# Optimization experiments

Measured on AMD Instinct MI355X. Metric: run time of the kernel, lower is better.

Reference implementation:

```python
import jax, jax.numpy as jnp
import numpy as np

B, L, DIN = 16, 1024, 512
H, DH = 4, 128          # num_heads = 4, head_dim = in_features // 4
DEG = 16                # avg random in-degree (plus one self-loop per node)
NEG_SLOPE = 0.2         # DGL GATConv default leaky_relu slope


def setup_inputs() -> dict:
    key = jax.random.key(0)
    ks = jax.random.split(key, 8)
    N = B * L
    E = N * DEG
    src = jax.random.randint(ks[0], (E,), 0, N)
    dst = jax.random.randint(ks[1], (E,), 0, N)
    loops = jnp.arange(N)
    src = jnp.concatenate([src, loops])  # self-loops guarantee every dst has in-edges
    dst = jnp.concatenate([dst, loops])
    s = 1.0 / np.sqrt(DIN)
    text = jax.random.normal(ks[2], (B, L, DIN), jnp.float32)
    weight = jax.random.normal(ks[3], (DIN, DIN), jnp.float32) * s      # module's self.weight
    fc_w = jax.random.normal(ks[4], (DIN, H * DH), jnp.float32) * s     # GATConv fc (no bias)
    attn_l = jax.random.normal(ks[5], (H, DH), jnp.float32) * s
    attn_r = jax.random.normal(ks[6], (H, DH), jnp.float32) * s
    bias = jax.random.normal(ks[7], (DIN,), jnp.float32) * 0.01         # module's self.bias
    return {"text": text, "weight": weight, "fc_w": fc_w,
            "attn_l": attn_l, "attn_r": attn_r, "bias": bias,
            "src": src, "dst": dst}


def reference(text, weight, fc_w, attn_l, attn_r, bias, src, dst):
    b, l, d = text.shape
    N = b * l
    # outer linear projection
    hidden = jnp.einsum('bld,de->ble', text, weight)
    feat = hidden.reshape(N, d)
    # GATConv: fc projection to heads
    h = (feat @ fc_w).reshape(N, H, DH)                 # [N, H, DH]
    el = jnp.einsum('nhd,hd->nh', h, attn_l)            # [N, H]
    er = jnp.einsum('nhd,hd->nh', h, attn_r)            # [N, H]
    # edge attention logits (src contributes el, dst contributes er)
    e = jax.nn.leaky_relu(el[src] + er[dst], NEG_SLOPE)  # [E, H]
    # segment (per-destination) softmax, numerically stable
    emax = jax.ops.segment_max(e, dst, num_segments=N)   # [N, H]
    ex = jnp.exp(e - emax[dst])
    denom = jax.ops.segment_sum(ex, dst, num_segments=N)
    alpha = ex / denom[dst]                              # [E, H]
    # weighted message aggregation (scatter-add)
    m = h[src] * alpha[:, :, None]                       # [E, H, DH]
    out = jax.ops.segment_sum(m, dst, num_segments=N)    # [N, H, DH]
    return out.reshape(b, l, H * DH) + bias
```

## Files before the change

kernel.cpp:

```cpp
#include <hip/hip_runtime.h>
#include <stdint.h>

#define AS1 __attribute__((address_space(1)))
#define AS3 __attribute__((address_space(3)))

typedef __attribute__((ext_vector_type(8))) short short8;
typedef __attribute__((ext_vector_type(4))) float f32x4;

#define CAP 64
#define NGEMM 512
#define NSCAT 128

__device__ __forceinline__ short f2bf(float f) {
  union { float f; unsigned u; } v; v.f = f;
  unsigned r = v.u + 0x7fffu + ((v.u >> 16) & 1u);
  return (short)(r >> 16);
}
__device__ __forceinline__ float bf_lo(unsigned w) { union { unsigned u; float f; } v; v.u = w << 16;          return v.f; }
__device__ __forceinline__ float bf_hi(unsigned w) { union { unsigned u; float f; } v; v.u = w & 0xffff0000u;  return v.f; }

__global__ __launch_bounds__(256) void k_w2t(const float* __restrict__ W,
                                             const float* __restrict__ F,
                                             short* __restrict__ W2t,
                                             int* __restrict__ cnt) {
  const int tid = threadIdx.x;
  const int b   = blockIdx.x;
  if (tid < 64) cnt[b * 64 + tid] = 0;

  __shared__ float sW[64][36];
  __shared__ float sF[64][36];
  const int bx = b & 15, by = b >> 4;
  const int d0 = bx * 32, j0 = by * 32;
  const int dx = tid & 15, jy = tid >> 4;
  float a00 = 0.f, a01 = 0.f, a10 = 0.f, a11 = 0.f;
  const int wr = tid >> 3, wc = (tid & 7) * 8;
  const int fr = tid >> 2, fc = (tid & 3) * 8;
  for (int e0 = 0; e0 < 512; e0 += 64) {
    float4 w0 = *(const float4*)&W[(size_t)(d0 + wr) * 512 + e0 + wc];
    float4 w1 = *(const float4*)&W[(size_t)(d0 + wr) * 512 + e0 + wc + 4];
    float4 f0 = *(const float4*)&F[(size_t)(e0 + fr) * 512 + j0 + fc];
    float4 f1 = *(const float4*)&F[(size_t)(e0 + fr) * 512 + j0 + fc + 4];
    sW[wc + 0][wr] = w0.x; sW[wc + 1][wr] = w0.y; sW[wc + 2][wr] = w0.z; sW[wc + 3][wr] = w0.w;
    sW[wc + 4][wr] = w1.x; sW[wc + 5][wr] = w1.y; sW[wc + 6][wr] = w1.z; sW[wc + 7][wr] = w1.w;
    *(float4*)&sF[fr][fc] = f0;
    *(float4*)&sF[fr][fc + 4] = f1;
    __syncthreads();
#pragma unroll
    for (int e = 0; e < 64; ++e) {
      float2 w2 = *(const float2*)&sW[e][dx * 2];
      float2 f2 = *(const float2*)&sF[e][jy * 2];
      a00 += w2.x * f2.x; a01 += w2.x * f2.y;
      a10 += w2.y * f2.x; a11 += w2.y * f2.y;
    }
    __syncthreads();
  }
  short* o0 = W2t + (size_t)(j0 + jy * 2) * 512 + d0 + dx * 2;
  o0[0] = f2bf(a00); o0[1] = f2bf(a10);
  o0[512] = f2bf(a01); o0[513] = f2bf(a11);
}

__global__ __launch_bounds__(256) void k_gemm_scatter(const float* __restrict__ A32,
                                                      const short* __restrict__ Bt,
                                                      short* __restrict__ Cs,
                                                      float* __restrict__ el,
                                                      float* __restrict__ er,
                                                      const float* __restrict__ attn_l,
                                                      const float* __restrict__ attn_r,
                                                      const int* __restrict__ src,
                                                      const int* __restrict__ dst,
                                                      int* __restrict__ cnt,
                                                      int* __restrict__ bucket,
                                                      int E, int N) {
  const int tid = threadIdx.x;
  if (blockIdx.x >= NGEMM) {
    for (int e = (blockIdx.x - NGEMM) * 256 + tid; e < E; e += NSCAT * 256) {
      int d = dst[e];
      int p = atomicAdd(&cnt[d], 1);
      if (p < CAP) bucket[(size_t)d * CAP + p] = src[e];
    }
    return;
  }

  __shared__ __align__(16) short sA[2][128 * 64];
  __shared__ __align__(16) short sB[2][128 * 64];
  __shared__ float sEl[128][2];
  __shared__ float sEr[128][2];
  const int bx   = blockIdx.x;
  const int xcd  = bx & 7, kk = bx >> 3;
  const int bm0  = (xcd * 16 + (kk & 15)) * 128;
  const int hh   = kk >> 4;
  const int bn0  = hh * 128;
  const int lane = tid & 63;
  const int wid  = tid >> 6;
  const int wm   = wid >> 1;
  const int wn   = wid & 1;
  const int cc   = lane & 15;

  f32x4 acc[4][4] = {};

  const int srow  = tid >> 3;
  const int sslot = (tid & 7) ^ (srow & 7);
  const int lslot = tid & 7;
  const int arow  = tid >> 1;
  const int ahalf = tid & 1;

  float4 f[2][8];

#define LOAD_A(SET, KT)                                                              \
  {                                                                                  \
    const float4* gA = (const float4*)(A32 + (size_t)(bm0 + arow) * 512 + (KT) * 64 + ahalf * 32); \
    _Pragma("unroll")                                                                \
    for (int s = 0; s < 8; ++s) f[SET][s] = gA[s];                                   \
  }

#define WRITE_A(SET, BUF)                                                            \
  {                                                                                  \
    _Pragma("unroll")                                                                \
    for (int s = 0; s < 4; ++s) {                                                    \
      short8 v;                                                                      \
      v[0] = f2bf(f[SET][2 * s].x); v[1] = f2bf(f[SET][2 * s].y);                    \
      v[2] = f2bf(f[SET][2 * s].z); v[3] = f2bf(f[SET][2 * s].w);                    \
      v[4] = f2bf(f[SET][2 * s + 1].x); v[5] = f2bf(f[SET][2 * s + 1].y);            \
      v[6] = f2bf(f[SET][2 * s + 1].z); v[7] = f2bf(f[SET][2 * s + 1].w);            \
      int slot = (ahalf * 4 + s) ^ (arow & 7);                                       \
      *(short8*)((BUF) + arow * 64 + slot * 8) = v;                                  \
    }                                                                                \
  }

#define STAGE_B(KT, BUF)                                                             \
  {                                                                                  \
    _Pragma("unroll")                                                                \
    for (int r = 0; r < 4; ++r) {                                                    \
      int row = r * 32 + srow;                                                       \
      __builtin_amdgcn_global_load_lds(                                              \
          (const AS1 void*)(Bt + (size_t)(bn0 + row) * 512 + (KT) * 64 + sslot * 8), \
          (AS3 void*)((BUF) + row * 64 + lslot * 8), 16, 0, 0);                      \
    }                                                                                \
  }

  LOAD_A(0, 0)
  LOAD_A(1, 1)
  STAGE_B(0, sB[0])
  WRITE_A(0, sA[0])
  __syncthreads();

#pragma unroll
  for (int kt = 0; kt < 8; ++kt) {
    const int cur = kt & 1;
    if (kt < 7) STAGE_B(kt + 1, sB[cur ^ 1])
    if (kt < 6) LOAD_A(kt & 1, kt + 2)
#pragma unroll
    for (int ks = 0; ks < 2; ++ks) {
      short8 af[4], bfr[4];
#pragma unroll
      for (int i = 0; i < 4; ++i) {
        int row  = wm * 64 + i * 16 + cc;
        int slot = (ks * 4 + (lane >> 4)) ^ (row & 7);
        af[i] = *(const short8*)(sA[cur] + row * 64 + slot * 8);
      }
#pragma unroll
      for (int j = 0; j < 4; ++j) {
        int row  = wn * 64 + j * 16 + cc;
        int slot = (ks * 4 + (lane >> 4)) ^ (row & 7);
        bfr[j] = *(const short8*)(sB[cur] + row * 64 + slot * 8);
      }
#pragma unroll
      for (int i = 0; i < 4; ++i)
#pragma unroll
        for (int j = 0; j < 4; ++j)
          acc[i][j] = __builtin_amdgcn_mfma_f32_16x16x32_bf16(af[i], bfr[j], acc[i][j], 0, 0, 0);
    }
    if (kt < 7) WRITE_A((kt + 1) & 1, sA[cur ^ 1])
    __syncthreads();
  }

  const int r4 = (lane >> 4) * 4;
#pragma unroll
  for (int i = 0; i < 4; ++i)
#pragma unroll
    for (int j = 0; j < 4; ++j) {
      int cin = wn * 64 + j * 16 + cc;
#pragma unroll
      for (int rg = 0; rg < 4; ++rg) {
        int gr = bm0 + wm * 64 + i * 16 + r4 + rg;
        Cs[((size_t)hh * N + gr) * 128 + cin] = f2bf(acc[i][j][rg]);
      }
    }
  float alv[4], arv[4];
#pragma unroll
  for (int j = 0; j < 4; ++j) {
    int cl = wn * 64 + j * 16 + cc;
    alv[j] = attn_l[hh * 128 + cl];
    arv[j] = attn_r[hh * 128 + cl];
  }
#pragma unroll
  for (int i = 0; i < 4; ++i)
#pragma unroll
    for (int rg = 0; rg < 4; ++rg) {
      float pl = 0.f, pr = 0.f;
#pragma unroll
      for (int j = 0; j < 4; ++j) {
        float v = acc[i][j][rg];
        pl += v * alv[j]; pr += v * arv[j];
      }
#pragma unroll
      for (int d = 1; d < 16; d <<= 1) {
        pl += __shfl_xor(pl, d);
        pr += __shfl_xor(pr, d);
      }
      if (cc == 0) {
        int row = wm * 64 + i * 16 + r4 + rg;
        sEl[row][wn] = pl;
        sEr[row][wn] = pr;
      }
    }
  __syncthreads();
  if (tid < 128) {
    int gr = bm0 + tid;
    el[gr * 4 + hh] = sEl[tid][0] + sEl[tid][1];
    er[gr * 4 + hh] = sEr[tid][0] + sEr[tid][1];
  }
}

__global__ __launch_bounds__(256) void k_aggregate(const int* __restrict__ cnt, const int* __restrict__ bucket,
                                                   const float* __restrict__ el, const float* __restrict__ er,
                                                   const short* __restrict__ hs, const float* __restrict__ bias,
                                                   float* __restrict__ out, int N) {
  const int b    = blockIdx.x;
  const int s    = (b >> 1) & 3;
  const int nt   = (b >> 3) * 2 + (b & 1);
  const int nd   = nt * 4 + (threadIdx.x >> 6);
  const int lane = threadIdx.x & 63;
  const int g    = lane >> 4;
  const int cl   = lane & 15;

  int n = cnt[nd]; n = (n < CAP) ? n : CAP;
  const int* bk = bucket + (size_t)nd * CAP;

  int l   = (lane < n) ? lane : (n - 1);
  int idx = bk[l];
  float ern = er[nd * 4 + s];
  float x = el[idx * 4 + s] + ern;
  x = (x > 0.f) ? x : 0.2f * x;
  float wgt = (lane < n) ? __expf(x) : 0.f;
  float ssum = wgt;
#pragma unroll
  for (int d = 1; d < 64; d <<= 1) ssum += __shfl_xor(ssum, d);

  const short* hbase = hs + (size_t)s * N * 128;
  float acc[8];
#pragma unroll
  for (int j = 0; j < 8; ++j) acc[j] = 0.f;

  for (int base = 0; base < n; base += 8) {
    int e0 = base + g, e1 = base + 4 + g;
    int s0 = __shfl(idx, e0), s1 = __shfl(idx, e1);
    float w0 = __shfl(wgt, e0), w1 = __shfl(wgt, e1);
    uint4 v0 = ((const uint4*)(hbase + (size_t)s0 * 128))[cl];
    uint4 v1 = ((const uint4*)(hbase + (size_t)s1 * 128))[cl];
    acc[0] += w0 * bf_lo(v0.x) + w1 * bf_lo(v1.x);
    acc[1] += w0 * bf_hi(v0.x) + w1 * bf_hi(v1.x);
    acc[2] += w0 * bf_lo(v0.y) + w1 * bf_lo(v1.y);
    acc[3] += w0 * bf_hi(v0.y) + w1 * bf_hi(v1.y);
    acc[4] += w0 * bf_lo(v0.z) + w1 * bf_lo(v1.z);
    acc[5] += w0 * bf_hi(v0.z) + w1 * bf_hi(v1.z);
    acc[6] += w0 * bf_lo(v0.w) + w1 * bf_lo(v1.w);
    acc[7] += w0 * bf_hi(v0.w) + w1 * bf_hi(v1.w);
  }

#pragma unroll
  for (int d = 16; d < 64; d <<= 1) {
#pragma unroll
    for (int j = 0; j < 8; ++j) acc[j] += __shfl_xor(acc[j], d);
  }

  if (g == 0) {
    float inv = 1.f / ssum;
    int c0 = s * 128 + cl * 8;
    float4 b0 = *(const float4*)(bias + c0);
    float4 b1 = *(const float4*)(bias + c0 + 4);
    float4 o0, o1;
    o0.x = acc[0] * inv + b0.x; o0.y = acc[1] * inv + b0.y;
    o0.z = acc[2] * inv + b0.z; o0.w = acc[3] * inv + b0.w;
    o1.x = acc[4] * inv + b1.x; o1.y = acc[5] * inv + b1.y;
    o1.z = acc[6] * inv + b1.z; o1.w = acc[7] * inv + b1.w;
    float* op = out + (size_t)nd * 512 + c0;
    *(float4*)op = o0;
    *(float4*)(op + 4) = o1;
  }
}

extern "C" void kernel_launch(void* const* d_in, const int* in_sizes, int n_in,
                              void* d_out, int out_size, void* d_ws, size_t ws_size,
                              hipStream_t stream) {
  const float* text   = (const float*)d_in[0];
  const float* weight = (const float*)d_in[1];
  const float* fcw    = (const float*)d_in[2];
  const float* attn_l = (const float*)d_in[3];
  const float* attn_r = (const float*)d_in[4];
  const float* bias   = (const float*)d_in[5];
  const int*   src    = (const int*)d_in[6];
  const int*   dst    = (const int*)d_in[7];
  const int E = in_sizes[6];
  const int N = in_sizes[0] / 512;

  char* ws = (char*)d_ws;
  size_t o = 0;
  auto carve = [&](size_t bytes) { void* p = ws + o; o = (o + bytes + 255) & ~(size_t)255; return p; };
  short* w2t    = (short*)carve((size_t)512 * 512 * 2);
  short* hs     = (short*)carve((size_t)N * 512 * 2);
  float* el     = (float*)carve((size_t)N * 4 * 4);
  float* er     = (float*)carve((size_t)N * 4 * 4);
  int*   cnt    = (int*)carve((size_t)N * 4);
  int*   bucket = (int*)carve((size_t)N * CAP * 4);

  k_w2t<<<256, 256, 0, stream>>>(weight, fcw, w2t, cnt);
  k_gemm_scatter<<<NGEMM + NSCAT, 256, 0, stream>>>(text, w2t, hs, el, er, attn_l, attn_r,
                                                    src, dst, cnt, bucket, E, N);
  k_aggregate<<<N * 4 / 4, 256, 0, stream>>>(cnt, bucket, el, er, hs, bias, (float*)d_out, N);
}
```

Before: 90.79 us.

## Split scatter from GEMM and halve GEMM K-tile to 32

Moves the edge-bucketing scatter out of the fused GEMM launch into its own kernel, launched on the same stream before the GEMM. The GEMM K-tile shrinks from 64 to 32 with 16 iterations, a new XOR swizzle, and simpler block-to-tile mapping without XCD-aware remapping. Smaller LDS footprint may raise occupancy, but the change loses the concurrent overlap of scatter with GEMM and adds a launch plus more barriers per tile.

```diff
diff --git a/kernel.cpp b/kernel.cpp
--- a/kernel.cpp
+++ b/kernel.cpp
@@ -8,8 +8,6 @@
 typedef __attribute__((ext_vector_type(4))) float f32x4;
 
 #define CAP 64
-#define NGEMM 512
-#define NSCAT 128
 
 __device__ __forceinline__ short f2bf(float f) {
   union { float f; unsigned u; } v; v.f = f;
@@ -59,36 +57,31 @@
   o0[512] = f2bf(a01); o0[513] = f2bf(a11);
 }
 
-__global__ __launch_bounds__(256) void k_gemm_scatter(const float* __restrict__ A32,
-                                                      const short* __restrict__ Bt,
-                                                      short* __restrict__ Cs,
-                                                      float* __restrict__ el,
-                                                      float* __restrict__ er,
-                                                      const float* __restrict__ attn_l,
-                                                      const float* __restrict__ attn_r,
-                                                      const int* __restrict__ src,
-                                                      const int* __restrict__ dst,
-                                                      int* __restrict__ cnt,
-                                                      int* __restrict__ bucket,
-                                                      int E, int N) {
-  const int tid = threadIdx.x;
-  if (blockIdx.x >= NGEMM) {
-    for (int e = (blockIdx.x - NGEMM) * 256 + tid; e < E; e += NSCAT * 256) {
-      int d = dst[e];
-      int p = atomicAdd(&cnt[d], 1);
-      if (p < CAP) bucket[(size_t)d * CAP + p] = src[e];
-    }
-    return;
-  }
-
-  __shared__ __align__(16) short sA[2][128 * 64];
-  __shared__ __align__(16) short sB[2][128 * 64];
+__global__ __launch_bounds__(256) void k_scatter(const int* __restrict__ src, const int* __restrict__ dst,
+                                                 int* __restrict__ cnt, int* __restrict__ bucket, int E) {
+  for (int e = blockIdx.x * 256 + threadIdx.x; e < E; e += 256 * 256) {
+    int d = dst[e];
+    int p = atomicAdd(&cnt[d], 1);
+    if (p < CAP) bucket[(size_t)d * CAP + p] = src[e];
+  }
+}
+
+__global__ __launch_bounds__(256) void k_gemm(const float* __restrict__ A32,
+                                              const short* __restrict__ Bt,
+                                              short* __restrict__ Cs,
+                                              float* __restrict__ el,
+                                              float* __restrict__ er,
+                                              const float* __restrict__ attn_l,
+                                              const float* __restrict__ attn_r,
+                                              int N) {
+  __shared__ __align__(16) short sA[2][128 * 32];
+  __shared__ __align__(16) short sB[2][128 * 32];
   __shared__ float sEl[128][2];
   __shared__ float sEr[128][2];
+  const int tid  = threadIdx.x;
   const int bx   = blockIdx.x;
-  const int xcd  = bx & 7, kk = bx >> 3;
-  const int bm0  = (xcd * 16 + (kk & 15)) * 128;
-  const int hh   = kk >> 4;
+  const int bm0  = (bx >> 2) * 128;
+  const int hh   = bx & 3;
   const int bn0  = hh * 128;
   const int lane = tid & 63;
   const int wid  = tid >> 6;
@@ -98,43 +91,43 @@
 
   f32x4 acc[4][4] = {};
 
-  const int srow  = tid >> 3;
-  const int sslot = (tid & 7) ^ (srow & 7);
-  const int lslot = tid & 7;
+  const int brow   = tid >> 2;
+  const int bs_src = (tid & 3) ^ ((tid >> 3) & 3);
+  const int bs_lin = tid & 3;
   const int arow  = tid >> 1;
   const int ahalf = tid & 1;
 
-  float4 f[2][8];
+  float4 f[2][4];
 
 #define LOAD_A(SET, KT)                                                              \
   {                                                                                  \
-    const float4* gA = (const float4*)(A32 + (size_t)(bm0 + arow) * 512 + (KT) * 64 + ahalf * 32); \
+    const float4* gA = (const float4*)(A32 + (size_t)(bm0 + arow) * 512 + (KT) * 32 + ahalf * 16); \
     _Pragma("unroll")                                                                \
-    for (int s = 0; s < 8; ++s) f[SET][s] = gA[s];                                   \
+    for (int s = 0; s < 4; ++s) f[SET][s] = gA[s];                                   \
   }
 
 #define WRITE_A(SET, BUF)                                                            \
   {                                                                                  \
     _Pragma("unroll")                                                                \
-    for (int s = 0; s < 4; ++s) {                                                    \
+    for (int s = 0; s < 2; ++s) {                                                    \
       short8 v;                                                                      \
       v[0] = f2bf(f[SET][2 * s].x); v[1] = f2bf(f[SET][2 * s].y);                    \
       v[2] = f2bf(f[SET][2 * s].z); v[3] = f2bf(f[SET][2 * s].w);                    \
       v[4] = f2bf(f[SET][2 * s + 1].x); v[5] = f2bf(f[SET][2 * s + 1].y);            \
       v[6] = f2bf(f[SET][2 * s + 1].z); v[7] = f2bf(f[SET][2 * s + 1].w);            \
-      int slot = (ahalf * 4 + s) ^ (arow & 7);                                       \
-      *(short8*)((BUF) + arow * 64 + slot * 8) = v;                                  \
+      int slot = (ahalf * 2 + s) ^ ((arow >> 1) & 3);                                \
+      *(short8*)((BUF) + arow * 32 + slot * 8) = v;                                  \
     }                                                                                \
   }
 
 #define STAGE_B(KT, BUF)                                                             \
   {                                                                                  \
     _Pragma("unroll")                                                                \
-    for (int r = 0; r < 4; ++r) {                                                    \
-      int row = r * 32 + srow;                                                       \
+    for (int r = 0; r < 2; ++r) {                                                    \
+      int row = r * 64 + brow;                                                       \
       __builtin_amdgcn_global_load_lds(                                              \
-          (const AS1 void*)(Bt + (size_t)(bn0 + row) * 512 + (KT) * 64 + sslot * 8), \
-          (AS3 void*)((BUF) + row * 64 + lslot * 8), 16, 0, 0);                      \
+          (const AS1 void*)(Bt + (size_t)(bn0 + row) * 512 + (KT) * 32 + bs_src * 8),\
+          (AS3 void*)((BUF) + row * 32 + bs_lin * 8), 16, 0, 0);                     \
     }                                                                                \
   }
 
@@ -145,32 +138,29 @@
   __syncthreads();
 
 #pragma unroll
-  for (int kt = 0; kt < 8; ++kt) {
+  for (int kt = 0; kt < 16; ++kt) {
     const int cur = kt & 1;
-    if (kt < 7) STAGE_B(kt + 1, sB[cur ^ 1])
-    if (kt < 6) LOAD_A(kt & 1, kt + 2)
-#pragma unroll
-    for (int ks = 0; ks < 2; ++ks) {
-      short8 af[4], bfr[4];
-#pragma unroll
-      for (int i = 0; i < 4; ++i) {
-        int row  = wm * 64 + i * 16 + cc;
-        int slot = (ks * 4 + (lane >> 4)) ^ (row & 7);
-        af[i] = *(const short8*)(sA[cur] + row * 64 + slot * 8);
-      }
-#pragma unroll
-      for (int j = 0; j < 4; ++j) {
-        int row  = wn * 64 + j * 16 + cc;
-        int slot = (ks * 4 + (lane >> 4)) ^ (row & 7);
-        bfr[j] = *(const short8*)(sB[cur] + row * 64 + slot * 8);
-      }
-#pragma unroll
-      for (int i = 0; i < 4; ++i)
-#pragma unroll
-        for (int j = 0; j < 4; ++j)
-          acc[i][j] = __builtin_amdgcn_mfma_f32_16x16x32_bf16(af[i], bfr[j], acc[i][j], 0, 0, 0);
-    }
-    if (kt < 7) WRITE_A((kt + 1) & 1, sA[cur ^ 1])
+    if (kt < 15) STAGE_B(kt + 1, sB[cur ^ 1])
+    if (kt < 14) LOAD_A(kt & 1, kt + 2)
+    short8 af[4], bfr[4];
+#pragma unroll
+    for (int i = 0; i < 4; ++i) {
+      int row  = wm * 64 + i * 16 + cc;
+      int slot = (lane >> 4) ^ ((row >> 1) & 3);
+      af[i] = *(const short8*)(sA[cur] + row * 32 + slot * 8);
+    }
+#pragma unroll
+    for (int j = 0; j < 4; ++j) {
+      int row  = wn * 64 + j * 16 + cc;
+      int slot = (lane >> 4) ^ ((row >> 1) & 3);
+      bfr[j] = *(const short8*)(sB[cur] + row * 32 + slot * 8);
+    }
+#pragma unroll
+    for (int i = 0; i < 4; ++i)
+#pragma unroll
+      for (int j = 0; j < 4; ++j)
+        acc[i][j] = __builtin_amdgcn_mfma_f32_16x16x32_bf16(af[i], bfr[j], acc[i][j], 0, 0, 0);
+    if (kt < 15) WRITE_A((kt + 1) & 1, sA[cur ^ 1])
     __syncthreads();
   }
 
@@ -315,7 +305,7 @@
   int*   bucket = (int*)carve((size_t)N * CAP * 4);
 
   k_w2t<<<256, 256, 0, stream>>>(weight, fcw, w2t, cnt);
-  k_gemm_scatter<<<NGEMM + NSCAT, 256, 0, stream>>>(text, w2t, hs, el, er, attn_l, attn_r,
-                                                    src, dst, cnt, bucket, E, N);
+  k_scatter<<<256, 256, 0, stream>>>(src, dst, cnt, bucket, E);
+  k_gemm<<<512, 256, 0, stream>>>(text, w2t, hs, el, er, attn_l, attn_r, N);
   k_aggregate<<<N * 4 / 4, 256, 0, stream>>>(cnt, bucket, el, er, hs, bias, (float*)d_out, N);
 }
```

Measured after the change: 98.73 us. 8.8% more time.
